# Optimization experiments

Measured on AMD Instinct MI355X. Metric: run time of the kernel, lower is better.

The kernel has to match this reference:

```python
import jax, jax.numpy as jnp
import numpy as np

D_MODEL = 1024
NHEAD = 16
D_K = D_MODEL // NHEAD
D_CHUNK = 128


def setup_inputs() -> dict:
    key = jax.random.key(0)
    ks = jax.random.split(key, 11)
    B, S = 4, 8192
    s = 1.0 / np.sqrt(D_MODEL)
    inp = {
        "q": jax.random.normal(ks[0], (B, S, D_MODEL), jnp.float32),
        "k": jax.random.normal(ks[1], (B, S, D_MODEL), jnp.float32),
        "v": jax.random.normal(ks[2], (B, S, D_MODEL), jnp.float32),
        "W_Q": jax.random.normal(ks[3], (D_MODEL, D_MODEL), jnp.float32) * s,
        "b_Q": jnp.zeros((D_MODEL,), jnp.float32),
        "W_K": jax.random.normal(ks[4], (D_MODEL, D_MODEL), jnp.float32) * s,
        "b_K": jnp.zeros((D_MODEL,), jnp.float32),
        "W_V": jax.random.normal(ks[5], (D_MODEL, D_MODEL), jnp.float32) * s,
        "b_V": jnp.zeros((D_MODEL,), jnp.float32),
        "W_O": jax.random.normal(ks[6], (D_MODEL, D_MODEL), jnp.float32) * s,
        "b_O": jnp.zeros((D_MODEL,), jnp.float32),
    }
    return inp


def reference(q, k, v, W_Q, b_Q, W_K, b_K, W_V, b_V, W_O, b_O):
    B, S, _ = q.shape
    C = S // D_CHUNK  # number of chunks

    def split_heads(x):
        # [B,S,D] -> [B,H,C,P,dk]  (matches view+transpose+view in torch)
        x = x.reshape(B, S, NHEAD, D_K).transpose(0, 2, 1, 3)
        return x.reshape(B, NHEAD, C, D_CHUNK, D_K)

    Q = split_heads(q @ W_Q.T + b_Q)
    K = split_heads(k @ W_K.T + b_K)
    V = split_heads(v @ W_V.T + b_V)

    # block-diagonal local attention: each [P,P] score matrix per (b,h,chunk)
    scores = jnp.einsum("bhcpd,bhcqd->bhcpq", Q, K) / np.sqrt(D_K).astype(jnp.float32)
    attn_w = jax.nn.softmax(scores, axis=-1)
    attn = jnp.einsum("bhcpq,bhcqd->bhcpd", attn_w, V)  # [B,H,C,P,dk]

    # Faithful to torch: attn.transpose(1,2).view(B,-1,d_model)
    # i.e. flatten [C,H,P,dk] contiguously into rows of d_model.
    concat = attn.transpose(0, 2, 1, 3, 4).reshape(B, S, D_MODEL)
    return concat @ W_O.T + b_O
```

## Files before the change

kernel.cpp:

```cpp
#include <hip/hip_runtime.h>
#include <hip/hip_bf16.h>


typedef __attribute__((ext_vector_type(8))) short short8;
typedef __attribute__((ext_vector_type(4))) float f32x4;
typedef __attribute__((ext_vector_type(4))) unsigned short us4;

__device__ __forceinline__ unsigned short f2bf(float f) {
  unsigned u = __float_as_uint(f);
  u += 0x7fffu + ((u >> 16) & 1u);
  return (unsigned short)(u >> 16);
}

__device__ __forceinline__ void gload16(const void* g, void* l) {
  __builtin_amdgcn_global_load_lds((const __attribute__((address_space(1))) void*)g,
                                   (__attribute__((address_space(3))) void*)l, 16, 0, 0);
}

__global__ void f2b4_kernel(const float* __restrict__ i0, const float* __restrict__ i1,
                            const float* __restrict__ i2, const float* __restrict__ i3,
                            unsigned short* __restrict__ o0, unsigned short* __restrict__ o1,
                            unsigned short* __restrict__ o2, unsigned short* __restrict__ o3,
                            int n) {
  const int z = blockIdx.z;
  const float* in = z == 0 ? i0 : z == 1 ? i1 : z == 2 ? i2 : i3;
  unsigned short* out = z == 0 ? o0 : z == 1 ? o1 : z == 2 ? o2 : o3;
  int i = (blockIdx.x * 256 + threadIdx.x) * 4;
  if (i >= n) return;
  f32x4 x = *(const f32x4*)(in + i);
  us4 o;
  #pragma unroll
  for (int j = 0; j < 4; ++j) o[j] = f2bf(x[j]);
  *(us4*)(out + i) = o;
}

__global__ __launch_bounds__(256)
void cvt3_kernel(const float* __restrict__ i0, const float* __restrict__ i1,
                 const float* __restrict__ i2, unsigned short* __restrict__ o0,
                 unsigned short* __restrict__ o1, unsigned short* __restrict__ o2, int n) {
  const int z = blockIdx.z;
  const float* in = z == 0 ? i0 : z == 1 ? i1 : i2;
  unsigned short* out = z == 0 ? o0 : z == 1 ? o1 : o2;
  int stride = gridDim.x * 256 * 8;
  for (int i = (blockIdx.x * 256 + threadIdx.x) * 8; i < n; i += stride) {
    f32x4 a = *(const f32x4*)(in + i);
    f32x4 b = *(const f32x4*)(in + i + 4);
    short8 o;
    #pragma unroll
    for (int j = 0; j < 4; ++j) {
      o[j]     = (short)f2bf(a[j]);
      o[4 + j] = (short)f2bf(b[j]);
    }
    *(short8*)(out + i) = o;
  }
}

template<bool C_F32>
__device__ __forceinline__ void gemm_core(const unsigned short* __restrict__ Ap,
                                          const unsigned short* __restrict__ Bp,
                                          const float* __restrict__ bias,
                                          void* __restrict__ Cp) {
  constexpr int BK = 64, NT = 16;
  const int tid = threadIdx.x;
  const int lane = tid & 63, wave = tid >> 6;
  const int lg = lane >> 4, li = lane & 15;
  const int wr = wave >> 2, wc = wave & 3;

  const int orig = blockIdx.y * 4 + blockIdx.x;
  const int wg = (orig & 7) * 64 + (orig >> 3);
  const int bn = wg & 3, bm = wg >> 2;

  const long arow0 = (long)bm * 256;
  const int bcol0 = bn * 256;

  __shared__ __align__(16) unsigned short As[2][256 * BK];
  __shared__ __align__(16) unsigned short Bs[2][256 * BK];

  float bv[4];
  #pragma unroll
  for (int n = 0; n < 4; ++n) bv[n] = bias[bcol0 + wc * 64 + n * 16 + li];

  f32x4 acc[8][4];
  #pragma unroll
  for (int m = 0; m < 8; ++m)
    #pragma unroll
    for (int n = 0; n < 4; ++n) acc[m][n] = (f32x4){0.f, 0.f, 0.f, 0.f};

  auto stage_half = [&](int u, int h) {
    const int k0 = u * BK;
    const int half = h & 1;
    unsigned short* dst = (h < 2 ? As[u & 1] : Bs[u & 1]) + half * (128 * BK);
    const unsigned short* src = (h < 2) ? Ap : Bp;
    const long rbase = (h < 2) ? (arow0 + half * 128) : (long)(bcol0 + half * 128);
    #pragma unroll
    for (int it = 0; it < 2; ++it) {
      int s = it * 512 + tid;
      int row = s >> 3;
      int eg = ((s & 7) ^ (row & 7)) * 8;
      gload16(src + (rbase + row) * 1024 + k0 + eg, (unsigned char*)dst + s * 16);
    }
  };

  stage_half(0, 0); stage_half(0, 1); stage_half(0, 2); stage_half(0, 3);
  stage_half(1, 2); stage_half(1, 3);
  asm volatile("s_waitcnt vmcnt(4)" ::: "memory");
  __builtin_amdgcn_sched_barrier(0);
  __builtin_amdgcn_s_barrier();

  for (int t = 0; t < NT; ++t) {
    const unsigned short* Asb = As[t & 1];
    const unsigned short* Bsb = Bs[t & 1];

    auto LDA = [&](int m, int kk) {
      return *(const short8*)(Asb + (wr * 128 + m * 16 + li) * BK +
                              (((kk * 4 + lg) ^ (li & 7)) * 8));
    };
    auto LDB = [&](int n, int kk) {
      return *(const short8*)(Bsb + (wc * 64 + n * 16 + li) * BK +
                              (((kk * 4 + lg) ^ (li & 7)) * 8));
    };

    short8 b0[4], b1[4];

    {
      short8 a0[4];
      #pragma unroll
      for (int i = 0; i < 4; ++i) a0[i] = LDA(i, 0);
      #pragma unroll
      for (int n = 0; n < 4; ++n) b0[n] = LDB(n, 0);
      if (t + 1 < NT) stage_half(t + 1, 0);
      __builtin_amdgcn_s_barrier();
      __builtin_amdgcn_s_setprio(1);
      #pragma unroll
      for (int i = 0; i < 4; ++i)
        #pragma unroll
        for (int n = 0; n < 4; ++n)
          acc[i][n] = __builtin_amdgcn_mfma_f32_16x16x32_bf16(a0[i], b0[n], acc[i][n], 0, 0, 0);
      __builtin_amdgcn_s_setprio(0);
      __builtin_amdgcn_s_barrier();
    }
    {
      short8 a1[4];
      #pragma unroll
      for (int i = 0; i < 4; ++i) a1[i] = LDA(i, 1);
      #pragma unroll
      for (int n = 0; n < 4; ++n) b1[n] = LDB(n, 1);
      if (t + 1 < NT) stage_half(t + 1, 1);
      __builtin_amdgcn_s_barrier();
      __builtin_amdgcn_s_setprio(1);
      #pragma unroll
      for (int i = 0; i < 4; ++i)
        #pragma unroll
        for (int n = 0; n < 4; ++n)
          acc[i][n] = __builtin_amdgcn_mfma_f32_16x16x32_bf16(a1[i], b1[n], acc[i][n], 0, 0, 0);
      __builtin_amdgcn_s_setprio(0);
      __builtin_amdgcn_s_barrier();
    }
    {
      short8 a2[4];
      #pragma unroll
      for (int i = 0; i < 4; ++i) a2[i] = LDA(4 + i, 0);
      if (t + 2 < NT) stage_half(t + 2, 2);
      __builtin_amdgcn_s_barrier();
      __builtin_amdgcn_s_setprio(1);
      #pragma unroll
      for (int i = 0; i < 4; ++i)
        #pragma unroll
        for (int n = 0; n < 4; ++n)
          acc[4 + i][n] = __builtin_amdgcn_mfma_f32_16x16x32_bf16(a2[i], b0[n], acc[4 + i][n], 0, 0, 0);
      __builtin_amdgcn_s_setprio(0);
      __builtin_amdgcn_s_barrier();
    }
    {
      short8 a3[4];
      #pragma unroll
      for (int i = 0; i < 4; ++i) a3[i] = LDA(4 + i, 1);
      if (t + 2 < NT) stage_half(t + 2, 3);
      if (t + 2 < NT) {
        asm volatile("s_waitcnt vmcnt(4)" ::: "memory");
      } else {
        asm volatile("s_waitcnt vmcnt(0)" ::: "memory");
      }
      __builtin_amdgcn_sched_barrier(0);
      __builtin_amdgcn_s_barrier();
      __builtin_amdgcn_s_setprio(1);
      #pragma unroll
      for (int i = 0; i < 4; ++i)
        #pragma unroll
        for (int n = 0; n < 4; ++n)
          acc[4 + i][n] = __builtin_amdgcn_mfma_f32_16x16x32_bf16(a3[i], b1[n], acc[4 + i][n], 0, 0, 0);
      __builtin_amdgcn_s_setprio(0);
      __builtin_amdgcn_s_barrier();
    }
  }

  float* wsc = (float*)As + wave * (16 * 68);
  #pragma unroll
  for (int m = 0; m < 8; ++m) {
    #pragma unroll
    for (int n = 0; n < 4; ++n)
      #pragma unroll
      for (int r = 0; r < 4; ++r)
        wsc[(lg * 4 + r) * 68 + n * 16 + li] = acc[m][n][r] + bv[n];
    asm volatile("s_waitcnt lgkmcnt(0)" ::: "memory");
    __builtin_amdgcn_sched_barrier(0);
    #pragma unroll
    for (int i = 0; i < 4; ++i) {
      int slot = i * 64 + lane;
      int r = slot >> 4, g = slot & 15;
      f32x4 vv = *(const f32x4*)(wsc + r * 68 + g * 4);
      long grow = arow0 + wr * 128 + m * 16 + r;
      long gcol = bcol0 + wc * 64 + g * 4;
      if constexpr (C_F32) {
        *(f32x4*)((float*)Cp + grow * 1024 + gcol) = vv;
      } else {
        us4 o;
        #pragma unroll
        for (int j = 0; j < 4; ++j) o[j] = f2bf(vv[j]);
        *(us4*)((unsigned short*)Cp + grow * 1024 + gcol) = o;
      }
    }
    asm volatile("s_waitcnt lgkmcnt(0)" ::: "memory");
    __builtin_amdgcn_sched_barrier(0);
  }
}

__global__ __launch_bounds__(512, 2)
void gemm_proj(const unsigned short* __restrict__ A0, const unsigned short* __restrict__ A1,
               const unsigned short* __restrict__ A2,
               const unsigned short* __restrict__ B0, const unsigned short* __restrict__ B1,
               const unsigned short* __restrict__ B2,
               const float* __restrict__ b0, const float* __restrict__ b1,
               const float* __restrict__ b2,
               unsigned short* __restrict__ C0, unsigned short* __restrict__ C1,
               unsigned short* __restrict__ C2) {
  const int z = blockIdx.z;
  const unsigned short* Ap = z == 0 ? A0 : z == 1 ? A1 : A2;
  const unsigned short* Bp = z == 0 ? B0 : z == 1 ? B1 : B2;
  const float* bias        = z == 0 ? b0 : z == 1 ? b1 : b2;
  unsigned short* Cp       = z == 0 ? C0 : z == 1 ? C1 : C2;
  gemm_core<false>(Ap, Bp, bias, Cp);
}

__global__ __launch_bounds__(512, 2)
void gemm_out(const unsigned short* __restrict__ Ap, const unsigned short* __restrict__ Bp,
              const float* __restrict__ bias, float* __restrict__ Cp) {
  gemm_core<true>(Ap, Bp, bias, Cp);
}

__global__ __launch_bounds__(256)
void attn_kernel(const unsigned short* __restrict__ Qp, const unsigned short* __restrict__ Kp,
                 const unsigned short* __restrict__ Vp, unsigned short* __restrict__ Cc) {
  const int bid = blockIdx.x;
  const int c = bid & 63, h = (bid >> 6) & 15, b = bid >> 10;
  const int tid = threadIdx.x;
  const int lane = tid & 63, wave = tid >> 6;
  const int lg = lane >> 4, li = lane & 15;

  __shared__ __align__(16) unsigned short Qs[128 * 64];
  __shared__ __align__(16) unsigned short Ks[128 * 64];
  __shared__ __align__(16) unsigned short Vs[128 * 64];
  __shared__ __align__(16) unsigned short Ps[4][32 * 128];

  const long base = ((long)(b * 8192 + c * 128)) * 1024 + h * 64;
  #pragma unroll
  for (int it = 0; it < 4; ++it) {
    int slot = it * 256 + tid;
    int row = slot >> 3, col = (slot & 7) * 8;
    long g = base + (long)row * 1024 + col;
    gload16(Qp + g, (unsigned char*)Qs + slot * 16);
    gload16(Kp + g, (unsigned char*)Ks + slot * 16);
    gload16(Vp + g, (unsigned char*)Vs + slot * 16);
  }
  __syncthreads();

  f32x4 sc[2][8];
  #pragma unroll
  for (int m = 0; m < 2; ++m)
    #pragma unroll
    for (int n = 0; n < 8; ++n) sc[m][n] = (f32x4){0.f, 0.f, 0.f, 0.f};

  short8 qf[2][2];
  #pragma unroll
  for (int m = 0; m < 2; ++m)
    #pragma unroll
    for (int ks = 0; ks < 2; ++ks)
      qf[m][ks] = *(const short8*)(Qs + (wave * 32 + m * 16 + li) * 64 + ks * 32 + lg * 8);

  #pragma unroll
  for (int n = 0; n < 8; ++n) {
    short8 kf0 = *(const short8*)(Ks + (n * 16 + li) * 64 + lg * 8);
    short8 kf1 = *(const short8*)(Ks + (n * 16 + li) * 64 + 32 + lg * 8);
    #pragma unroll
    for (int m = 0; m < 2; ++m) {
      sc[m][n] = __builtin_amdgcn_mfma_f32_16x16x32_bf16(qf[m][0], kf0, sc[m][n], 0, 0, 0);
      sc[m][n] = __builtin_amdgcn_mfma_f32_16x16x32_bf16(qf[m][1], kf1, sc[m][n], 0, 0, 0);
    }
  }

  #pragma unroll
  for (int m = 0; m < 2; ++m)
    #pragma unroll
    for (int r = 0; r < 4; ++r) {
      float mx = sc[m][0][r];
      #pragma unroll
      for (int n = 1; n < 8; ++n) mx = fmaxf(mx, sc[m][n][r]);
      #pragma unroll
      for (int d = 1; d < 16; d <<= 1) mx = fmaxf(mx, __shfl_xor(mx, d));
      float sum = 0.f;
      #pragma unroll
      for (int n = 0; n < 8; ++n) {
        float p = __expf((sc[m][n][r] - mx) * 0.125f);
        sc[m][n][r] = p;
        sum += p;
      }
      #pragma unroll
      for (int d = 1; d < 16; d <<= 1) sum += __shfl_xor(sum, d);
      float rinv = 1.f / sum;
      #pragma unroll
      for (int n = 0; n < 8; ++n) sc[m][n][r] *= rinv;
    }

  #pragma unroll
  for (int m = 0; m < 2; ++m)
    #pragma unroll
    for (int n = 0; n < 8; ++n)
      #pragma unroll
      for (int r = 0; r < 4; ++r)
        Ps[wave][(m * 16 + lg * 4 + r) * 128 + n * 16 + li] = f2bf(sc[m][n][r]);
  __syncthreads();

  f32x4 oc[2][4];
  #pragma unroll
  for (int m = 0; m < 2; ++m)
    #pragma unroll
    for (int n = 0; n < 4; ++n) oc[m][n] = (f32x4){0.f, 0.f, 0.f, 0.f};

  #pragma unroll
  for (int ks = 0; ks < 4; ++ks) {
    short8 vf[4];
    #pragma unroll
    for (int n = 0; n < 4; ++n)
      #pragma unroll
      for (int j = 0; j < 8; ++j)
        vf[n][j] = (short)Vs[(ks * 32 + lg * 8 + j) * 64 + n * 16 + li];
    #pragma unroll
    for (int m = 0; m < 2; ++m) {
      short8 pf = *(const short8*)(Ps[wave] + (m * 16 + li) * 128 + ks * 32 + lg * 8);
      #pragma unroll
      for (int n = 0; n < 4; ++n)
        oc[m][n] = __builtin_amdgcn_mfma_f32_16x16x32_bf16(pf, vf[n], oc[m][n], 0, 0, 0);
    }
  }

  #pragma unroll
  for (int m = 0; m < 2; ++m)
    #pragma unroll
    for (int n = 0; n < 4; ++n)
      #pragma unroll
      for (int r = 0; r < 4; ++r) {
        int p = wave * 32 + m * 16 + lg * 4 + r;
        int d = n * 16 + li;
        int s = c * 128 + h * 8 + (p >> 4);
        int colo = (p & 15) * 64 + d;
        Cc[((long)(b * 8192 + s)) * 1024 + colo] = f2bf(oc[m][n][r]);
      }
}

extern "C" void kernel_launch(void* const* d_in, const int* in_sizes, int n_in,
                              void* d_out, int out_size, void* d_ws, size_t ws_size,
                              hipStream_t stream) {
  (void)in_sizes; (void)n_in; (void)out_size; (void)ws_size;
  const float* q  = (const float*)d_in[0];
  const float* k  = (const float*)d_in[1];
  const float* v  = (const float*)d_in[2];
  const float* WQ = (const float*)d_in[3];
  const float* bQ = (const float*)d_in[4];
  const float* WK = (const float*)d_in[5];
  const float* bK = (const float*)d_in[6];
  const float* WV = (const float*)d_in[7];
  const float* bV = (const float*)d_in[8];
  const float* WO = (const float*)d_in[9];
  const float* bO = (const float*)d_in[10];

  const size_t MN = 32768ull * 1024ull;
  unsigned short* qb  = (unsigned short*)d_ws;
  unsigned short* kb  = qb + MN;
  unsigned short* vb  = kb + MN;
  unsigned short* Qp  = vb + MN;
  unsigned short* Kp  = Qp + MN;
  unsigned short* Vp  = Kp + MN;
  unsigned short* Cc  = Vp + MN;
  unsigned short* WQb = Cc + MN;
  unsigned short* WKb = WQb + (1 << 20);
  unsigned short* WVb = WKb + (1 << 20);
  unsigned short* WOb = WVb + (1 << 20);

  dim3 gw(1024, 1, 4);
  f2b4_kernel<<<gw, 256, 0, stream>>>(WQ, WK, WV, WO, WQb, WKb, WVb, WOb, 1 << 20);

  const int NA = (int)MN;
  dim3 gc(1024, 1, 3);
  cvt3_kernel<<<gc, 256, 0, stream>>>(q, k, v, qb, kb, vb, NA);

  dim3 gp(4, 128, 3);
  gemm_proj<<<gp, 512, 0, stream>>>(qb, kb, vb, WQb, WKb, WVb, bQ, bK, bV, Qp, Kp, Vp);

  attn_kernel<<<4096, 256, 0, stream>>>(Qp, Kp, Vp, Cc);

  dim3 go(4, 128);
  gemm_out<<<go, 512, 0, stream>>>(Cc, WOb, bO, (float*)d_out);
}
```

Baseline: 560.7 us.

## Fuse fp32-to-bf16 activation conversion into projection GEMM A-tile loading

Removes the separate cvt3 kernel that converted q/k/v to bf16 in workspace. The projection GEMM now loads fp32 A tiles into registers, converts them to bf16, and writes them to LDS inside the pipelined loop, while B tiles still use direct global-to-LDS loads. This avoids writing and rereading the bf16 copies of the activations and saves one launch. In exchange it adds register pressure from the fp32 staging buffers, doubles A-side global read width per tile, and changes the vmcnt-based synchronisation, which may weaken the overlap of loads and MFMA work.

```diff
diff --git a/kernel.cpp b/kernel.cpp
--- a/kernel.cpp
+++ b/kernel.cpp
@@ -34,29 +34,8 @@
   *(us4*)(out + i) = o;
 }
 
-__global__ __launch_bounds__(256)
-void cvt3_kernel(const float* __restrict__ i0, const float* __restrict__ i1,
-                 const float* __restrict__ i2, unsigned short* __restrict__ o0,
-                 unsigned short* __restrict__ o1, unsigned short* __restrict__ o2, int n) {
-  const int z = blockIdx.z;
-  const float* in = z == 0 ? i0 : z == 1 ? i1 : i2;
-  unsigned short* out = z == 0 ? o0 : z == 1 ? o1 : o2;
-  int stride = gridDim.x * 256 * 8;
-  for (int i = (blockIdx.x * 256 + threadIdx.x) * 8; i < n; i += stride) {
-    f32x4 a = *(const f32x4*)(in + i);
-    f32x4 b = *(const f32x4*)(in + i + 4);
-    short8 o;
-    #pragma unroll
-    for (int j = 0; j < 4; ++j) {
-      o[j]     = (short)f2bf(a[j]);
-      o[4 + j] = (short)f2bf(b[j]);
-    }
-    *(short8*)(out + i) = o;
-  }
-}
-
-template<bool C_F32>
-__device__ __forceinline__ void gemm_core(const unsigned short* __restrict__ Ap,
+template<bool A_F32, bool C_F32>
+__device__ __forceinline__ void gemm_core(const void* __restrict__ Apv,
                                           const unsigned short* __restrict__ Bp,
                                           const float* __restrict__ bias,
                                           void* __restrict__ Cp) {
@@ -66,6 +45,9 @@
   const int lg = lane >> 4, li = lane & 15;
   const int wr = wave >> 2, wc = wave & 3;
 
+  const unsigned short* Ab = (const unsigned short*)Apv;
+  const float* Af = (const float*)Apv;
+
   const int orig = blockIdx.y * 4 + blockIdx.x;
   const int wg = (orig & 7) * 64 + (orig >> 3);
   const int bn = wg & 3, bm = wg >> 2;
@@ -90,7 +72,7 @@
     const int k0 = u * BK;
     const int half = h & 1;
     unsigned short* dst = (h < 2 ? As[u & 1] : Bs[u & 1]) + half * (128 * BK);
-    const unsigned short* src = (h < 2) ? Ap : Bp;
+    const unsigned short* src = (h < 2) ? Ab : Bp;
     const long rbase = (h < 2) ? (arow0 + half * 128) : (long)(bcol0 + half * 128);
     #pragma unroll
     for (int it = 0; it < 2; ++it) {
@@ -101,11 +83,52 @@
     }
   };
 
-  stage_half(0, 0); stage_half(0, 1); stage_half(0, 2); stage_half(0, 3);
-  stage_half(1, 2); stage_half(1, 3);
-  asm volatile("s_waitcnt vmcnt(4)" ::: "memory");
-  __builtin_amdgcn_sched_barrier(0);
-  __builtin_amdgcn_s_barrier();
+  f32x4 areg[4][2];
+  auto issueA = [&](int u) {
+    #pragma unroll
+    for (int hf = 0; hf < 2; ++hf)
+      #pragma unroll
+      for (int it = 0; it < 2; ++it) {
+        int s = it * 512 + tid;
+        int row = s >> 3;
+        int ce = ((s & 7) ^ (row & 7)) * 8;
+        const float* p = Af + (arow0 + hf * 128 + row) * 1024 + u * BK + ce;
+        areg[hf * 2 + it][0] = *(const f32x4*)p;
+        areg[hf * 2 + it][1] = *(const f32x4*)(p + 4);
+      }
+  };
+  auto writeA = [&](int u) {
+    unsigned short* dstb = As[u & 1];
+    #pragma unroll
+    for (int hf = 0; hf < 2; ++hf)
+      #pragma unroll
+      for (int it = 0; it < 2; ++it) {
+        int s = it * 512 + tid;
+        short8 o;
+        #pragma unroll
+        for (int j = 0; j < 4; ++j) {
+          o[j]     = (short)f2bf(areg[hf * 2 + it][0][j]);
+          o[4 + j] = (short)f2bf(areg[hf * 2 + it][1][j]);
+        }
+        *(short8*)((unsigned char*)(dstb + hf * (128 * BK)) + s * 16) = o;
+      }
+    asm volatile("s_waitcnt lgkmcnt(0)" ::: "memory");
+    __builtin_amdgcn_sched_barrier(0);
+  };
+
+  if constexpr (A_F32) {
+    stage_half(0, 2); stage_half(0, 3);
+    issueA(0);
+    stage_half(1, 2); stage_half(1, 3);
+    writeA(0);
+    __builtin_amdgcn_s_barrier();
+  } else {
+    stage_half(0, 0); stage_half(0, 1); stage_half(0, 2); stage_half(0, 3);
+    stage_half(1, 2); stage_half(1, 3);
+    asm volatile("s_waitcnt vmcnt(4)" ::: "memory");
+    __builtin_amdgcn_sched_barrier(0);
+    __builtin_amdgcn_s_barrier();
+  }
 
   for (int t = 0; t < NT; ++t) {
     const unsigned short* Asb = As[t & 1];
@@ -128,7 +151,11 @@
       for (int i = 0; i < 4; ++i) a0[i] = LDA(i, 0);
       #pragma unroll
       for (int n = 0; n < 4; ++n) b0[n] = LDB(n, 0);
-      if (t + 1 < NT) stage_half(t + 1, 0);
+      if constexpr (A_F32) {
+        if (t + 1 < NT) issueA(t + 1);
+      } else {
+        if (t + 1 < NT) stage_half(t + 1, 0);
+      }
       __builtin_amdgcn_s_barrier();
       __builtin_amdgcn_s_setprio(1);
       #pragma unroll
@@ -145,7 +172,9 @@
       for (int i = 0; i < 4; ++i) a1[i] = LDA(i, 1);
       #pragma unroll
       for (int n = 0; n < 4; ++n) b1[n] = LDB(n, 1);
-      if (t + 1 < NT) stage_half(t + 1, 1);
+      if constexpr (!A_F32) {
+        if (t + 1 < NT) stage_half(t + 1, 1);
+      }
       __builtin_amdgcn_s_barrier();
       __builtin_amdgcn_s_setprio(1);
       #pragma unroll
@@ -161,6 +190,9 @@
       #pragma unroll
       for (int i = 0; i < 4; ++i) a2[i] = LDA(4 + i, 0);
       if (t + 2 < NT) stage_half(t + 2, 2);
+      if constexpr (A_F32) {
+        if (t + 1 < NT) writeA(t + 1);
+      }
       __builtin_amdgcn_s_barrier();
       __builtin_amdgcn_s_setprio(1);
       #pragma unroll
@@ -176,12 +208,14 @@
       #pragma unroll
       for (int i = 0; i < 4; ++i) a3[i] = LDA(4 + i, 1);
       if (t + 2 < NT) stage_half(t + 2, 3);
-      if (t + 2 < NT) {
-        asm volatile("s_waitcnt vmcnt(4)" ::: "memory");
-      } else {
-        asm volatile("s_waitcnt vmcnt(0)" ::: "memory");
-      }
-      __builtin_amdgcn_sched_barrier(0);
+      if constexpr (!A_F32) {
+        if (t + 2 < NT) {
+          asm volatile("s_waitcnt vmcnt(4)" ::: "memory");
+        } else {
+          asm volatile("s_waitcnt vmcnt(0)" ::: "memory");
+        }
+        __builtin_amdgcn_sched_barrier(0);
+      }
       __builtin_amdgcn_s_barrier();
       __builtin_amdgcn_s_setprio(1);
       #pragma unroll
@@ -226,8 +260,8 @@
 }
 
 __global__ __launch_bounds__(512, 2)
-void gemm_proj(const unsigned short* __restrict__ A0, const unsigned short* __restrict__ A1,
-               const unsigned short* __restrict__ A2,
+void gemm_proj(const float* __restrict__ A0, const float* __restrict__ A1,
+               const float* __restrict__ A2,
                const unsigned short* __restrict__ B0, const unsigned short* __restrict__ B1,
                const unsigned short* __restrict__ B2,
                const float* __restrict__ b0, const float* __restrict__ b1,
@@ -235,17 +269,17 @@
                unsigned short* __restrict__ C0, unsigned short* __restrict__ C1,
                unsigned short* __restrict__ C2) {
   const int z = blockIdx.z;
-  const unsigned short* Ap = z == 0 ? A0 : z == 1 ? A1 : A2;
+  const float* Ap          = z == 0 ? A0 : z == 1 ? A1 : A2;
   const unsigned short* Bp = z == 0 ? B0 : z == 1 ? B1 : B2;
   const float* bias        = z == 0 ? b0 : z == 1 ? b1 : b2;
   unsigned short* Cp       = z == 0 ? C0 : z == 1 ? C1 : C2;
-  gemm_core<false>(Ap, Bp, bias, Cp);
+  gemm_core<true, false>(Ap, Bp, bias, Cp);
 }
 
 __global__ __launch_bounds__(512, 2)
 void gemm_out(const unsigned short* __restrict__ Ap, const unsigned short* __restrict__ Bp,
               const float* __restrict__ bias, float* __restrict__ Cp) {
-  gemm_core<true>(Ap, Bp, bias, Cp);
+  gemm_core<false, true>(Ap, Bp, bias, Cp);
 }
 
 __global__ __launch_bounds__(256)
@@ -384,10 +418,7 @@
   const float* bO = (const float*)d_in[10];
 
   const size_t MN = 32768ull * 1024ull;
-  unsigned short* qb  = (unsigned short*)d_ws;
-  unsigned short* kb  = qb + MN;
-  unsigned short* vb  = kb + MN;
-  unsigned short* Qp  = vb + MN;
+  unsigned short* Qp  = (unsigned short*)d_ws;
   unsigned short* Kp  = Qp + MN;
   unsigned short* Vp  = Kp + MN;
   unsigned short* Cc  = Vp + MN;
@@ -399,12 +430,8 @@
   dim3 gw(1024, 1, 4);
   f2b4_kernel<<<gw, 256, 0, stream>>>(WQ, WK, WV, WO, WQb, WKb, WVb, WOb, 1 << 20);
 
-  const int NA = (int)MN;
-  dim3 gc(1024, 1, 3);
-  cvt3_kernel<<<gc, 256, 0, stream>>>(q, k, v, qb, kb, vb, NA);
-
   dim3 gp(4, 128, 3);
-  gemm_proj<<<gp, 512, 0, stream>>>(qb, kb, vb, WQb, WKb, WVb, bQ, bK, bV, Qp, Kp, Vp);
+  gemm_proj<<<gp, 512, 0, stream>>>(q, k, v, WQb, WKb, WVb, bQ, bK, bV, Qp, Kp, Vp);
 
   attn_kernel<<<4096, 256, 0, stream>>>(Qp, Kp, Vp, Cc);
 
```

Measured after the change: 559.9 us. No clear change (-0.1%).
